# Performance work log

Hardware: AMD Instinct MI355X
Metric: run time of the kernel (lower is better)

Reference implementation:

```python
import jax, jax.numpy as jnp
import numpy as np

N = 50000        # nodes
E = 800000       # edges (avg degree 16)
F_IN = 128       # input feature dim == heads*hidden of every layer
H = 4            # heads per layer
C = 32           # hidden (per-head out) per layer
ED = 16          # edge_dim
L = 3            # num GAT layers
NEG_SLOPE = 0.2  # PyG GATConv default


def setup_inputs() -> dict:
    key = jax.random.key(0)
    ks = jax.random.split(key, 13)
    s = 0.1
    x = jax.random.normal(ks[0], (N, F_IN), jnp.float32)
    edge_index = jax.random.randint(ks[1], (2, E), 0, N, dtype=jnp.int32)
    edge_attr = jax.random.normal(ks[2], (E, ED), jnp.float32)
    # stacked per-layer GATConv params (all layers are 128 -> 4x32)
    W_src = jax.random.normal(ks[3], (L, F_IN, H * C), jnp.float32) * s
    att_src = jax.random.normal(ks[4], (L, H, C), jnp.float32) * s
    att_dst = jax.random.normal(ks[5], (L, H, C), jnp.float32) * s
    W_edge = jax.random.normal(ks[6], (L, ED, H * C), jnp.float32) * s
    att_edge = jax.random.normal(ks[7], (L, H, C), jnp.float32) * s
    bias = jnp.zeros((L, H * C), jnp.float32)
    # dense head: Linear(128,256) -> ReLU -> Linear(256,2)
    W1 = jax.random.normal(ks[8], (H * C, 2 * H * C), jnp.float32) * s
    b1 = jnp.zeros((2 * H * C,), jnp.float32)
    W2 = jax.random.normal(ks[9], (2 * H * C, 2), jnp.float32) * s
    b2 = jnp.zeros((2,), jnp.float32)
    return {"x": x, "edge_index": edge_index, "edge_attr": edge_attr,
            "W_src": W_src, "att_src": att_src, "att_dst": att_dst,
            "W_edge": W_edge, "att_edge": att_edge, "bias": bias,
            "W1": W1, "b1": b1, "W2": W2, "b2": b2}


def reference(x, edge_index, edge_attr, W_src, att_src, att_dst,
              W_edge, att_edge, bias, W1, b1, W2, b2):
    src, dst = edge_index[0], edge_index[1]
    # add_self_loops with fill_value='mean': self-loop edge_attr = mean of
    # incoming edge attrs per node (0 if no incoming edges)
    deg = jax.ops.segment_sum(jnp.ones((E,), x.dtype), dst, num_segments=N)
    loop_attr = jax.ops.segment_sum(edge_attr, dst, num_segments=N) \
        / jnp.maximum(deg, 1.0)[:, None]
    nodes = jnp.arange(N, dtype=src.dtype)
    src_f = jnp.concatenate([src, nodes])          # [E+N]
    dst_f = jnp.concatenate([dst, nodes])          # [E+N]
    ea = jnp.concatenate([edge_attr, loop_attr], axis=0)  # [E+N, ED]

    h = x
    for l in range(L):
        hp = (h @ W_src[l]).reshape(N, H, C)                 # [N,H,C]
        a_s = (hp * att_src[l]).sum(-1)                      # [N,H]
        a_d = (hp * att_dst[l]).sum(-1)                      # [N,H]
        ef = (ea @ W_edge[l]).reshape(-1, H, C)              # [E+N,H,C]
        a_e = (ef * att_edge[l]).sum(-1)                     # [E+N,H]
        alpha = jax.nn.leaky_relu(a_s[src_f] + a_d[dst_f] + a_e, NEG_SLOPE)
        # segment softmax over destination node (self-loops ensure coverage)
        m = jax.ops.segment_max(alpha, dst_f, num_segments=N)
        ex = jnp.exp(alpha - m[dst_f])
        denom = jax.ops.segment_sum(ex, dst_f, num_segments=N)
        w = ex / denom[dst_f]                                # [E+N,H]
        agg = jax.ops.segment_sum(w[:, :, None] * hp[src_f], dst_f,
                                  num_segments=N)            # [N,H,C]
        h = jax.nn.relu(agg.reshape(N, H * C) + bias[l])

    g = h.mean(axis=0, keepdims=True)                        # batch=None -> [1,128]
    hid = jax.nn.relu(g @ W1 + b1)
    return hid @ W2 + b2                                     # [1,2]
```

## Files before the change

### kernel.cpp

```cpp
#include <hip/hip_runtime.h>
#include <math.h>

#define N_NODES 50000
#define N_EDGES 800000
#define F 128
#define H 4
#define C 32
#define ED 16
#define L 3
#define NEG 0.2f
#define ET (N_EDGES + N_NODES)
#define SCAN_B ((N_NODES + 255) / 256)


__global__ void k_count(const int* __restrict__ dst, int* __restrict__ deg) {
    int e = blockIdx.x * 256 + threadIdx.x;
    if (e < N_EDGES) atomicAdd(&deg[dst[e]], 1);
}

__global__ __launch_bounds__(256) void k_scanA(const int* __restrict__ deg,
                                               int* __restrict__ off, int* __restrict__ bsum) {
    __shared__ int sh[256];
    int t = threadIdx.x;
    int i = blockIdx.x * 256 + t;
    int v = (i < N_NODES) ? (deg[i] + 1) : 0;
    sh[t] = v;
    __syncthreads();
    #pragma unroll
    for (int d = 1; d < 256; d <<= 1) {
        int u = (t >= d) ? sh[t - d] : 0;
        __syncthreads();
        sh[t] += u;
        __syncthreads();
    }
    if (i < N_NODES) off[i] = sh[t] - v;
    if (t == 255) bsum[blockIdx.x] = sh[255];
}

__global__ __launch_bounds__(256) void k_scanB(const int* __restrict__ bsum,
                                               int* __restrict__ boff, int* __restrict__ off) {
    __shared__ int sh[256];
    int t = threadIdx.x;
    int v = (t < SCAN_B) ? bsum[t] : 0;
    sh[t] = v;
    __syncthreads();
    #pragma unroll
    for (int d = 1; d < 256; d <<= 1) {
        int u = (t >= d) ? sh[t - d] : 0;
        __syncthreads();
        sh[t] += u;
        __syncthreads();
    }
    if (t < SCAN_B) boff[t] = sh[t] - v;
    if (t == 255) off[N_NODES] = sh[255];
}

__global__ void k_scanC(int* __restrict__ off, const int* __restrict__ boff) {
    int i = blockIdx.x * 256 + threadIdx.x;
    if (i < N_NODES) off[i] += boff[blockIdx.x];
}

__global__ void k_scatter(const int* __restrict__ ei, const int* __restrict__ off,
                          int* __restrict__ cursor, int* __restrict__ src_csr,
                          int* __restrict__ eid_csr) {
    int e = blockIdx.x * 256 + threadIdx.x;
    if (e < N_EDGES) {
        int d = ei[N_EDGES + e];
        int p = atomicAdd(&cursor[d], 1);
        int slot = off[d] + p;
        src_csr[slot] = ei[e];
        eid_csr[slot] = e;
    } else if (e < ET) {
        int nn = e - N_EDGES;
        int p = atomicAdd(&cursor[nn], 1);
        int slot = off[nn] + p;
        src_csr[slot] = nn;
        eid_csr[slot] = e;
    }
}

__global__ void k_we2(const float* __restrict__ W_edge, const float* __restrict__ att_edge,
                      float* __restrict__ we2) {
    int idx = blockIdx.x * 64 + threadIdx.x;
    if (idx >= L * ED * H) return;
    int l = idx / (ED * H);
    int r = idx % (ED * H);
    int d = r / H, h = r % H;
    float s = 0.f;
    for (int c = 0; c < C; c++)
        s += W_edge[(size_t)(l * ED + d) * (H * C) + h * C + c] * att_edge[(l * H + h) * C + c];
    we2[idx] = s;
}


#define BM 64
#define BK 32
__global__ __launch_bounds__(256) void k_gemm(const float* __restrict__ A,
                                              const float* __restrict__ W,
                                              const float* __restrict__ att_src_l,
                                              const float* __restrict__ att_dst_l,
                                              float* __restrict__ Out,
                                              float* __restrict__ a_s,
                                              float* __restrict__ a_d) {
    __shared__ float As[BM][BK + 1];
    __shared__ float Bs[BK][F];
    int block_row = blockIdx.x * BM;
    int t = threadIdx.x;
    int tx = t & 31;
    int ty = t >> 5;
    float acc[8][4] = {};
    for (int k0 = 0; k0 < F; k0 += BK) {
        #pragma unroll
        for (int i = 0; i < 2; i++) {
            int idx = t + i * 256;
            int r = idx >> 3, cq = idx & 7;
            int gr = block_row + r;
            float4 v = make_float4(0.f, 0.f, 0.f, 0.f);
            if (gr < N_NODES) v = *(const float4*)&A[(size_t)gr * F + k0 + cq * 4];
            As[r][cq * 4 + 0] = v.x; As[r][cq * 4 + 1] = v.y;
            As[r][cq * 4 + 2] = v.z; As[r][cq * 4 + 3] = v.w;
        }
        #pragma unroll
        for (int i = 0; i < 4; i++) {
            int idx = t + i * 256;
            int r = idx >> 5, cq = idx & 31;
            float4 v = *(const float4*)&W[(size_t)(k0 + r) * F + cq * 4];
            *(float4*)&Bs[r][cq * 4] = v;
        }
        __syncthreads();
        for (int kk = 0; kk < BK; kk++) {
            float b[4];
            #pragma unroll
            for (int j = 0; j < 4; j++) b[j] = Bs[kk][tx + 32 * j];
            #pragma unroll
            for (int i = 0; i < 8; i++) {
                float a = As[ty * 8 + i][kk];
                #pragma unroll
                for (int j = 0; j < 4; j++) acc[i][j] += a * b[j];
            }
        }
        __syncthreads();
    }
    float avs[4], avd[4];
    #pragma unroll
    for (int j = 0; j < 4; j++) {
        avs[j] = att_src_l[j * 32 + tx];
        avd[j] = att_dst_l[j * 32 + tx];
    }
    #pragma unroll
    for (int i = 0; i < 8; i++) {
        int gr = block_row + ty * 8 + i;
        bool ok = (gr < N_NODES);
        if (ok) {
            #pragma unroll
            for (int j = 0; j < 4; j++) Out[(size_t)gr * F + tx + 32 * j] = acc[i][j];
        }
        #pragma unroll
        for (int j = 0; j < 4; j++) {
            float vs = acc[i][j] * avs[j];
            float vd = acc[i][j] * avd[j];
            #pragma unroll
            for (int m = 1; m < 32; m <<= 1) {
                vs += __shfl_xor(vs, m, 64);
                vd += __shfl_xor(vd, m, 64);
            }
            if (tx == 0 && ok) {
                a_s[gr * H + j] = vs;
                a_d[gr * H + j] = vd;
            }
        }
    }
}

__global__ __launch_bounds__(256) void k_alpha(const int* __restrict__ eid_csr,
                                               const int* __restrict__ src_csr,
                                               const int* __restrict__ off,
                                               const float* __restrict__ edge_attr,
                                               const float* __restrict__ we2l,
                                               const float* __restrict__ a_s,
                                               const float* __restrict__ a_d,
                                               float* __restrict__ alpha_csr) {
    int n = blockIdx.x * 4 + (threadIdx.x >> 6);
    if (n >= N_NODES) return;
    int lane = threadIdx.x & 63;
    int beg = off[n], end = off[n + 1];
    float4 w[ED];
    #pragma unroll
    for (int k = 0; k < ED; k++) w[k] = *(const float4*)&we2l[k * 4];
    float4 adn = *(const float4*)&a_d[(size_t)n * 4];
    float sx = 0.f, sy = 0.f, sz = 0.f, sw = 0.f;
    int self_slot = -1;
    for (int i = beg + lane; i < end; i += 64) {
        int eid = eid_csr[i];
        if (eid < N_EDGES) {
            int src = src_csr[i];
            float4 asrc = *(const float4*)&a_s[(size_t)src * 4];
            const float* ea = &edge_attr[(size_t)eid * ED];
            float eav[ED];
            #pragma unroll
            for (int q = 0; q < ED / 4; q++) {
                float4 v = *(const float4*)&ea[q * 4];
                eav[q * 4 + 0] = v.x; eav[q * 4 + 1] = v.y;
                eav[q * 4 + 2] = v.z; eav[q * 4 + 3] = v.w;
            }
            float ax = 0.f, ay = 0.f, az = 0.f, aw = 0.f;
            #pragma unroll
            for (int k = 0; k < ED; k++) {
                float v = eav[k];
                ax += v * w[k].x; ay += v * w[k].y;
                az += v * w[k].z; aw += v * w[k].w;
            }
            sx += ax; sy += ay; sz += az; sw += aw;
            float4 o;
            o.x = asrc.x + adn.x + ax; o.x = (o.x > 0.f) ? o.x : NEG * o.x;
            o.y = asrc.y + adn.y + ay; o.y = (o.y > 0.f) ? o.y : NEG * o.y;
            o.z = asrc.z + adn.z + az; o.z = (o.z > 0.f) ? o.z : NEG * o.z;
            o.w = asrc.w + adn.w + aw; o.w = (o.w > 0.f) ? o.w : NEG * o.w;
            *(float4*)&alpha_csr[(size_t)i * H] = o;
        } else {
            self_slot = i;
        }
    }
    #pragma unroll
    for (int m = 1; m < 64; m <<= 1) {
        sx += __shfl_xor(sx, m, 64);
        sy += __shfl_xor(sy, m, 64);
        sz += __shfl_xor(sz, m, 64);
        sw += __shfl_xor(sw, m, 64);
    }
    if (self_slot >= 0) {
        float inv = 1.f / fmaxf((float)(end - beg - 1), 1.f);
        float4 asn = *(const float4*)&a_s[(size_t)n * 4];
        float4 o;
        o.x = asn.x + adn.x + sx * inv; o.x = (o.x > 0.f) ? o.x : NEG * o.x;
        o.y = asn.y + adn.y + sy * inv; o.y = (o.y > 0.f) ? o.y : NEG * o.y;
        o.z = asn.z + adn.z + sz * inv; o.z = (o.z > 0.f) ? o.z : NEG * o.z;
        o.w = asn.w + adn.w + sw * inv; o.w = (o.w > 0.f) ? o.w : NEG * o.w;
        *(float4*)&alpha_csr[(size_t)self_slot * H] = o;
    }
}

__global__ __launch_bounds__(128) void k_agg(const int* __restrict__ src_csr, const int* __restrict__ off,
                                             const float* __restrict__ alpha_csr,
                                             const float* __restrict__ hp, const float* __restrict__ bias_l,
                                             float* __restrict__ hout) {
    int n = blockIdx.x;
    int c = threadIdx.x;
    int h = c >> 5;
    int beg = off[n], end = off[n + 1];
    float acc0 = 0.f, acc1 = 0.f, acc2 = 0.f, acc3 = 0.f;
    float den0 = 0.f, den1 = 0.f, den2 = 0.f, den3 = 0.f;
    int i = beg;
    for (; i + 4 <= end; i += 4) {
        int s0 = src_csr[i], s1 = src_csr[i + 1], s2 = src_csr[i + 2], s3 = src_csr[i + 3];
        float a0 = alpha_csr[(size_t)i * H + h];
        float a1 = alpha_csr[(size_t)(i + 1) * H + h];
        float a2 = alpha_csr[(size_t)(i + 2) * H + h];
        float a3 = alpha_csr[(size_t)(i + 3) * H + h];
        float e0 = __expf(a0), e1 = __expf(a1), e2 = __expf(a2), e3 = __expf(a3);
        acc0 += e0 * hp[(size_t)s0 * F + c];
        acc1 += e1 * hp[(size_t)s1 * F + c];
        acc2 += e2 * hp[(size_t)s2 * F + c];
        acc3 += e3 * hp[(size_t)s3 * F + c];
        den0 += e0; den1 += e1; den2 += e2; den3 += e3;
    }
    for (; i < end; i++) {
        int s0 = src_csr[i];
        float a0 = alpha_csr[(size_t)i * H + h];
        float e0 = __expf(a0);
        acc0 += e0 * hp[(size_t)s0 * F + c];
        den0 += e0;
    }
    float acc = (acc0 + acc1) + (acc2 + acc3);
    float den = (den0 + den1) + (den2 + den3);
    float v = acc / den + bias_l[c];
    hout[(size_t)n * F + c] = fmaxf(v, 0.f);
}


__global__ void k_pool(const float* __restrict__ hfinal, float* __restrict__ gsum) {
    int c = threadIdx.x;
    float s = 0.f;
    for (int n = blockIdx.x; n < N_NODES; n += gridDim.x)
        s += hfinal[(size_t)n * F + c];
    atomicAdd(&gsum[c], s);
}

__global__ __launch_bounds__(256) void k_mlp(const float* __restrict__ gsum, const float* __restrict__ W1,
                                             const float* __restrict__ b1, const float* __restrict__ W2,
                                             const float* __restrict__ b2, float* __restrict__ out) {
    __shared__ float g[F];
    __shared__ float hid[2 * F];
    __shared__ float red[256];
    int t = threadIdx.x;
    if (t < F) g[t] = gsum[t] * (1.0f / N_NODES);
    __syncthreads();
    float s = b1[t];
    for (int k = 0; k < F; k++) s += g[k] * W1[k * (2 * F) + t];
    hid[t] = fmaxf(s, 0.f);
    __syncthreads();
    for (int i = 0; i < 2; i++) {
        red[t] = hid[t] * W2[t * 2 + i];
        __syncthreads();
        for (int stp = 128; stp > 0; stp >>= 1) {
            if (t < stp) red[t] += red[t + stp];
            __syncthreads();
        }
        if (t == 0) out[i] = red[0] + b2[i];
        __syncthreads();
    }
}


extern "C" void kernel_launch(void* const* d_in, const int* in_sizes, int n_in,
                              void* d_out, int out_size, void* d_ws, size_t ws_size,
                              hipStream_t stream) {
    const float* x        = (const float*)d_in[0];
    const int*   ei       = (const int*)d_in[1];
    const float* edge_attr= (const float*)d_in[2];
    const float* W_src    = (const float*)d_in[3];
    const float* att_src  = (const float*)d_in[4];
    const float* att_dst  = (const float*)d_in[5];
    const float* W_edge   = (const float*)d_in[6];
    const float* att_edge = (const float*)d_in[7];
    const float* bias     = (const float*)d_in[8];
    const float* W1       = (const float*)d_in[9];
    const float* b1       = (const float*)d_in[10];
    const float* W2       = (const float*)d_in[11];
    const float* b2       = (const float*)d_in[12];
    float* out = (float*)d_out;

    char* p = (char*)d_ws;
    auto alloc = [&](size_t bytes) -> char* {
        char* r = p;
        p += (bytes + 255) & ~(size_t)255;
        return r;
    };
    int*      deg      = (int*)alloc((size_t)N_NODES * 4);
    int*      cursor   = (int*)alloc((size_t)N_NODES * 4);
    int*      off      = (int*)alloc((size_t)(N_NODES + 1) * 4);
    int*      bsum     = (int*)alloc((size_t)SCAN_B * 4);
    int*      boff     = (int*)alloc((size_t)SCAN_B * 4);
    int*      src_csr  = (int*)alloc((size_t)ET * 4);
    int*      eid_csr  = (int*)alloc((size_t)ET * 4);
    float*    we2      = (float*)alloc((size_t)L * ED * H * 4);
    float*    a_s      = (float*)alloc((size_t)N_NODES * H * 4);
    float*    a_d      = (float*)alloc((size_t)N_NODES * H * 4);
    float*    alpha_csr= (float*)alloc((size_t)ET * H * 4);
    float*    hp       = (float*)alloc((size_t)N_NODES * F * 4);
    float*    hA       = (float*)alloc((size_t)N_NODES * F * 4);
    float*    hB       = (float*)alloc((size_t)N_NODES * F * 4);
    float*    gsum     = (float*)alloc((size_t)F * 4);

    hipMemsetAsync(deg, 0, (size_t)N_NODES * 4, stream);
    hipMemsetAsync(cursor, 0, (size_t)N_NODES * 4, stream);
    hipMemsetAsync(gsum, 0, (size_t)F * 4, stream);

    const int* dst = ei + N_EDGES;
    k_count<<<(N_EDGES + 255) / 256, 256, 0, stream>>>(dst, deg);
    k_scanA<<<SCAN_B, 256, 0, stream>>>(deg, off, bsum);
    k_scanB<<<1, 256, 0, stream>>>(bsum, boff, off);
    k_scanC<<<SCAN_B, 256, 0, stream>>>(off, boff);
    k_scatter<<<(ET + 255) / 256, 256, 0, stream>>>(ei, off, cursor, src_csr, eid_csr);
    k_we2<<<3, 64, 0, stream>>>(W_edge, att_edge, we2);

    const float* hin = x;
    float* houts[3] = {hA, hB, hA};
    for (int l = 0; l < L; l++) {
        k_gemm<<<(N_NODES + BM - 1) / BM, 256, 0, stream>>>(hin, W_src + (size_t)l * F * F,
                                                            att_src + l * H * C, att_dst + l * H * C,
                                                            hp, a_s, a_d);
        k_alpha<<<(N_NODES + 3) / 4, 256, 0, stream>>>(eid_csr, src_csr, off, edge_attr,
                                                       we2 + l * ED * H, a_s, a_d, alpha_csr);
        k_agg<<<N_NODES, 128, 0, stream>>>(src_csr, off, alpha_csr, hp,
                                           bias + l * F, houts[l]);
        hin = houts[l];
    }
    k_pool<<<256, 128, 0, stream>>>(hA, gsum);
    k_mlp<<<1, 256, 0, stream>>>(gsum, W1, b1, W2, b2, out);
}
```

Measured before the change: 681.7 us.

## Store projected node features in bf16 and aggregate one node per wavefront

The GEMM now writes the projected features hp as bf16 instead of fp32, which halves the bytes gathered per edge in the aggregation kernel. The aggregation kernel is restructured so that one 64-lane wavefront handles a node, with each lane loading two bf16 channels. Four nodes share a 256-thread block instead of one node per 128-thread block. This cuts random-gather bandwidth and block count, but drops the features to bf16 precision, which may affect accuracy across three layers.

```diff
diff --git a/kernel.cpp b/kernel.cpp
--- a/kernel.cpp
+++ b/kernel.cpp
@@ -11,6 +11,17 @@
 #define NEG 0.2f
 #define ET (N_EDGES + N_NODES)
 #define SCAN_B ((N_NODES + 255) / 256)
+
+typedef unsigned short bf16_t;
+
+__device__ __forceinline__ bf16_t f2bf(float f) {
+    unsigned u = __float_as_uint(f);
+    unsigned r = (u + 0x7fffu + ((u >> 16) & 1u)) >> 16;
+    return (bf16_t)r;
+}
+__device__ __forceinline__ float bf2f(bf16_t b) {
+    return __uint_as_float(((unsigned)b) << 16);
+}
 
 
 __global__ void k_count(const int* __restrict__ dst, int* __restrict__ deg) {
@@ -99,7 +110,7 @@
                                               const float* __restrict__ W,
                                               const float* __restrict__ att_src_l,
                                               const float* __restrict__ att_dst_l,
-                                              float* __restrict__ Out,
+                                              bf16_t* __restrict__ hpb,
                                               float* __restrict__ a_s,
                                               float* __restrict__ a_d) {
     __shared__ float As[BM][BK + 1];
@@ -153,7 +164,7 @@
         bool ok = (gr < N_NODES);
         if (ok) {
             #pragma unroll
-            for (int j = 0; j < 4; j++) Out[(size_t)gr * F + tx + 32 * j] = acc[i][j];
+            for (int j = 0; j < 4; j++) hpb[(size_t)gr * F + tx + 32 * j] = f2bf(acc[i][j]);
         }
         #pragma unroll
         for (int j = 0; j < 4; j++) {
@@ -240,15 +251,17 @@
     }
 }
 
-__global__ __launch_bounds__(128) void k_agg(const int* __restrict__ src_csr, const int* __restrict__ off,
+__global__ __launch_bounds__(256) void k_agg(const int* __restrict__ src_csr, const int* __restrict__ off,
                                              const float* __restrict__ alpha_csr,
-                                             const float* __restrict__ hp, const float* __restrict__ bias_l,
+                                             const bf16_t* __restrict__ hpb, const float* __restrict__ bias_l,
                                              float* __restrict__ hout) {
-    int n = blockIdx.x;
-    int c = threadIdx.x;
-    int h = c >> 5;
+    int n = blockIdx.x * 4 + (threadIdx.x >> 6);
+    if (n >= N_NODES) return;
+    int lane = threadIdx.x & 63;
+    int h = lane >> 4;
     int beg = off[n], end = off[n + 1];
-    float acc0 = 0.f, acc1 = 0.f, acc2 = 0.f, acc3 = 0.f;
+    float accA0 = 0.f, accA1 = 0.f, accA2 = 0.f, accA3 = 0.f;
+    float accB0 = 0.f, accB1 = 0.f, accB2 = 0.f, accB3 = 0.f;
     float den0 = 0.f, den1 = 0.f, den2 = 0.f, den3 = 0.f;
     int i = beg;
     for (; i + 4 <= end; i += 4) {
@@ -257,24 +270,33 @@
         float a1 = alpha_csr[(size_t)(i + 1) * H + h];
         float a2 = alpha_csr[(size_t)(i + 2) * H + h];
         float a3 = alpha_csr[(size_t)(i + 3) * H + h];
+        ushort2 v0 = *(const ushort2*)&hpb[(size_t)s0 * F + 2 * lane];
+        ushort2 v1 = *(const ushort2*)&hpb[(size_t)s1 * F + 2 * lane];
+        ushort2 v2 = *(const ushort2*)&hpb[(size_t)s2 * F + 2 * lane];
+        ushort2 v3 = *(const ushort2*)&hpb[(size_t)s3 * F + 2 * lane];
         float e0 = __expf(a0), e1 = __expf(a1), e2 = __expf(a2), e3 = __expf(a3);
-        acc0 += e0 * hp[(size_t)s0 * F + c];
-        acc1 += e1 * hp[(size_t)s1 * F + c];
-        acc2 += e2 * hp[(size_t)s2 * F + c];
-        acc3 += e3 * hp[(size_t)s3 * F + c];
+        accA0 += e0 * bf2f(v0.x); accB0 += e0 * bf2f(v0.y);
+        accA1 += e1 * bf2f(v1.x); accB1 += e1 * bf2f(v1.y);
+        accA2 += e2 * bf2f(v2.x); accB2 += e2 * bf2f(v2.y);
+        accA3 += e3 * bf2f(v3.x); accB3 += e3 * bf2f(v3.y);
         den0 += e0; den1 += e1; den2 += e2; den3 += e3;
     }
     for (; i < end; i++) {
         int s0 = src_csr[i];
         float a0 = alpha_csr[(size_t)i * H + h];
+        ushort2 v0 = *(const ushort2*)&hpb[(size_t)s0 * F + 2 * lane];
         float e0 = __expf(a0);
-        acc0 += e0 * hp[(size_t)s0 * F + c];
+        accA0 += e0 * bf2f(v0.x); accB0 += e0 * bf2f(v0.y);
         den0 += e0;
     }
-    float acc = (acc0 + acc1) + (acc2 + acc3);
-    float den = (den0 + den1) + (den2 + den3);
-    float v = acc / den + bias_l[c];
-    hout[(size_t)n * F + c] = fmaxf(v, 0.f);
+    float accA = (accA0 + accA1) + (accA2 + accA3);
+    float accB = (accB0 + accB1) + (accB2 + accB3);
+    float den  = (den0 + den1) + (den2 + den3);
+    float2 bia = *(const float2*)&bias_l[2 * lane];
+    float2 o;
+    o.x = fmaxf(accA / den + bia.x, 0.f);
+    o.y = fmaxf(accB / den + bia.y, 0.f);
+    *(float2*)&hout[(size_t)n * F + 2 * lane] = o;
 }
 
 
@@ -347,7 +369,7 @@
     float*    a_s      = (float*)alloc((size_t)N_NODES * H * 4);
     float*    a_d      = (float*)alloc((size_t)N_NODES * H * 4);
     float*    alpha_csr= (float*)alloc((size_t)ET * H * 4);
-    float*    hp       = (float*)alloc((size_t)N_NODES * F * 4);
+    bf16_t*   hpb      = (bf16_t*)alloc((size_t)N_NODES * F * 2);
     float*    hA       = (float*)alloc((size_t)N_NODES * F * 4);
     float*    hB       = (float*)alloc((size_t)N_NODES * F * 4);
     float*    gsum     = (float*)alloc((size_t)F * 4);
@@ -369,11 +391,11 @@
     for (int l = 0; l < L; l++) {
         k_gemm<<<(N_NODES + BM - 1) / BM, 256, 0, stream>>>(hin, W_src + (size_t)l * F * F,
                                                             att_src + l * H * C, att_dst + l * H * C,
-                                                            hp, a_s, a_d);
+                                                            hpb, a_s, a_d);
         k_alpha<<<(N_NODES + 3) / 4, 256, 0, stream>>>(eid_csr, src_csr, off, edge_attr,
                                                        we2 + l * ED * H, a_s, a_d, alpha_csr);
-        k_agg<<<N_NODES, 128, 0, stream>>>(src_csr, off, alpha_csr, hp,
-                                           bias + l * F, houts[l]);
+        k_agg<<<(N_NODES + 3) / 4, 256, 0, stream>>>(src_csr, off, alpha_csr, hpb,
+                                                     bias + l * F, houts[l]);
         hin = houts[l];
     }
     k_pool<<<256, 128, 0, stream>>>(hA, gsum);
```

New measurement: 615.1 us. -9.8%, faster.
